# Performance work log

Hardware: AMD Instinct MI355X
Metric: run time of the kernel (lower is better)

## Reference

```python
import jax, jax.numpy as jnp
import numpy as np

B = 8192
EPS = 1e-5


def _bn(x, g, b):
    # BatchNorm1d in training mode: biased batch statistics
    m = jnp.mean(x, axis=0)
    v = jnp.mean((x - m) ** 2, axis=0)
    return g * (x - m) * jax.lax.rsqrt(v + EPS) + b


def setup_inputs() -> dict:
    key = jax.random.key(0)
    ks = jax.random.split(key, 24)
    w = lambda k, shape: jax.random.normal(k, shape, jnp.float32) * 0.02
    z = lambda shape: jnp.zeros(shape, jnp.float32)
    o = lambda shape: jnp.ones(shape, jnp.float32)
    inp = {"pred_vertices": jax.random.normal(ks[0], (B, 1723, 3), jnp.float32)}
    inp["W0"] = w(ks[1], (5169, 1024)); inp["b0"] = z(1024); inp["g0"] = o(1024); inp["be0"] = z(1024)
    inp["W1a"] = w(ks[2], (1024, 1024)); inp["b1a"] = z(1024); inp["g1a"] = o(1024); inp["be1a"] = z(1024)
    inp["W1b"] = w(ks[3], (1024, 1024)); inp["b1b"] = z(1024); inp["g1b"] = o(1024); inp["be1b"] = z(1024)
    inp["W2a"] = w(ks[4], (1024, 1024)); inp["b2a"] = z(1024); inp["g2a"] = o(1024); inp["be2a"] = z(1024)
    inp["W2b"] = w(ks[5], (1024, 1024)); inp["b2b"] = z(1024); inp["g2b"] = o(1024); inp["be2b"] = z(1024)
    inp["W3"] = w(ks[6], (1024, 226)); inp["b3"] = z(226)
    return inp


def reference(pred_vertices, W0, b0, g0, be0,
              W1a, b1a, g1a, be1a, W1b, b1b, g1b, be1b,
              W2a, b2a, g2a, be2a, W2b, b2b, g2b, be2b,
              W3, b3):
    bsz = pred_vertices.shape[0]
    x = pred_vertices.reshape(bsz, 1723 * 3)
    # FCBlock: Linear -> BN -> ReLU
    h = jax.nn.relu(_bn(x @ W0 + b0, g0, be0))
    # FCResBlock x2: relu(x + BN(Linear(relu(BN(Linear(x))))))
    t = jax.nn.relu(_bn(h @ W1a + b1a, g1a, be1a))
    t = _bn(t @ W1b + b1b, g1b, be1b)
    h = jax.nn.relu(h + t)
    t = jax.nn.relu(_bn(h @ W2a + b2a, g2a, be2a))
    t = _bn(t @ W2b + b2b, g2b, be2b)
    h = jax.nn.relu(h + t)
    out = h @ W3 + b3  # (B, 226)
    rot = out[:, :216].reshape(-1, 3, 3)  # (B*24, 3, 3)
    pred_betas = out[:, 216:]
    # Batched Procrustes orthogonalization: R = U V^T, then scale by det (no-grad)
    U, S, Vh = jnp.linalg.svd(rot, full_matrices=False)
    R = jnp.einsum('nij,njk->nik', U, Vh)
    det = jax.lax.stop_gradient(jnp.linalg.det(R))[:, None, None]
    pred_rotmat = (R * det).reshape(bsz, 24, 3, 3)
    return (pred_rotmat, pred_betas)
```

## Files before the change

kernel.cpp:

```cpp
#include <hip/hip_runtime.h>
#include <hip/hip_bf16.h>
#include <math.h>

typedef __attribute__((ext_vector_type(8))) _Float16 half8;
typedef __attribute__((ext_vector_type(4))) float floatx4;
typedef __attribute__((ext_vector_type(4))) unsigned short ushortx4;

__device__ __forceinline__ float hu2f(unsigned short u) {
    _Float16 h;
    __builtin_memcpy(&h, &u, 2);
    return (float)h;
}
__device__ __forceinline__ unsigned short f2hu(float x) {
    _Float16 h = (_Float16)x;
    unsigned short u;
    __builtin_memcpy(&u, &h, 2);
    return u;
}
__device__ __forceinline__ void split2(float a, unsigned short& s0,
                                       unsigned short& s1) {
    s0 = f2hu(a);
    float r1 = a - hu2f(s0);
    s1 = f2hu(r1);
}

typedef __attribute__((address_space(1))) unsigned int as1_u32;
typedef __attribute__((address_space(3))) unsigned int as3_u32;
__device__ __forceinline__ void gload16(const void* g, void* l) {
    __builtin_amdgcn_global_load_lds((const as1_u32*)g, (as3_u32*)l, 16, 0, 0);
}

__device__ __forceinline__ void wsplit_body(
    const float* __restrict__ W, unsigned short* __restrict__ out,
    int Ktrue, int Kpad, int Ntrue, int Nalloc, int k0, int n0,
    float (*T)[33], int tx, int ty)
{
#pragma unroll
    for (int i = 0; i < 4; i++) {
        int k = k0 + ty + 8 * i, n = n0 + tx;
        T[ty + 8 * i][tx] = (k < Ktrue && n < Ntrue) ? W[(size_t)k * Ntrue + n] : 0.f;
    }
    __syncthreads();
    const size_t PS = (size_t)Nalloc * Kpad;
#pragma unroll
    for (int i = 0; i < 4; i++) {
        int n = n0 + ty + 8 * i, k = k0 + tx;
        if (n < Nalloc) {
            unsigned short h0, h1;
            split2(T[tx][ty + 8 * i], h0, h1);
            size_t base = (size_t)n * Kpad + k;
            out[base] = h0;
            out[PS + base] = h1;
        }
    }
}

__global__ __launch_bounds__(256) void wsplit_all_kernel(
    const float* __restrict__ W0,  const float* __restrict__ W1a,
    const float* __restrict__ W1b, const float* __restrict__ W2a,
    const float* __restrict__ W2b, const float* __restrict__ W3,
    unsigned short* __restrict__ w0p,  unsigned short* __restrict__ w1ap,
    unsigned short* __restrict__ w1bp, unsigned short* __restrict__ w2ap,
    unsigned short* __restrict__ w2bp, unsigned short* __restrict__ w3p)
{
    __shared__ float T[32][33];
    const int tx = threadIdx.x & 31, ty = threadIdx.x >> 5;
    int bid = blockIdx.x;
    if (bid < 5184) {
        wsplit_body(W0, w0p, 5169, 5184, 1024, 1024,
                    (bid % 162) * 32, (bid / 162) * 32, T, tx, ty);
    } else if (bid < 6208) {
        int r = bid - 5184;
        wsplit_body(W1a, w1ap, 1024, 1024, 1024, 1024,
                    (r & 31) * 32, (r >> 5) * 32, T, tx, ty);
    } else if (bid < 7232) {
        int r = bid - 6208;
        wsplit_body(W1b, w1bp, 1024, 1024, 1024, 1024,
                    (r & 31) * 32, (r >> 5) * 32, T, tx, ty);
    } else if (bid < 8256) {
        int r = bid - 7232;
        wsplit_body(W2a, w2ap, 1024, 1024, 1024, 1024,
                    (r & 31) * 32, (r >> 5) * 32, T, tx, ty);
    } else if (bid < 9280) {
        int r = bid - 8256;
        wsplit_body(W2b, w2bp, 1024, 1024, 1024, 1024,
                    (r & 31) * 32, (r >> 5) * 32, T, tx, ty);
    } else {
        int r = bid - 9280;
        wsplit_body(W3, w3p, 1024, 1024, 226, 256,
                    (r & 31) * 32, (r >> 5) * 32, T, tx, ty);
    }
}

__global__ __launch_bounds__(256) void asplit2_kernel(
    const float* __restrict__ A, unsigned short* __restrict__ out,
    int Ka, int Kpad, int M)
{
    const int kq = Kpad >> 2;
    const int n = M * kq;
    int idx = blockIdx.x * 256 + threadIdx.x;
    if (idx >= n) return;
    int row = idx / kq, c4 = idx - row * kq;
    const size_t PS = (size_t)M * Kpad;
    ushortx4 o0, o1;
#pragma unroll
    for (int e = 0; e < 4; e++) {
        int col = c4 * 4 + e;
        float v = (col < Ka) ? A[(size_t)row * Ka + col] : 0.f;
        unsigned short a, b;
        split2(v, a, b);
        o0[e] = a; o1[e] = b;
    }
    size_t base = (size_t)row * Kpad + c4 * 4;
    *(ushortx4*)(out + base) = o0;
    *(ushortx4*)(out + PS + base) = o1;
}

__global__ __launch_bounds__(256, 3) void mfma_gemm_h(
    const unsigned short* __restrict__ Apl,
    const unsigned short* __restrict__ Bpl,
    const float* __restrict__ bias, float* __restrict__ C,
    float* __restrict__ part,
    int M, int N, int Kpad, int Nb)
{
    __shared__ __align__(16) unsigned short As[2][128][32];
    __shared__ __align__(16) unsigned short Bs[2][128][32];

    const int tid = threadIdx.x;
    const int lane = tid & 63;
    const int wave = tid >> 6;
    const int wm = (wave & 1) * 64, wn = (wave >> 1) * 64;

    const int gx = gridDim.x;
    const int nwg = gx * gridDim.y;
    const int id = blockIdx.y * gx + blockIdx.x;
    const int cpx = nwg >> 3;
    const int swz = (id & 7) * cpx + (id >> 3);
    const int bm = (swz / gx) * 128, bn = (swz % gx) * 128;

    const int l15 = lane & 15, q = lane >> 4;
    const size_t PSA = (size_t)M * Kpad;
    const size_t PSB = (size_t)Nb * Kpad;

    const int srow = lane >> 2;
    const int gslot = (lane & 3) ^ ((srow >> 1) & 3);
    const int rkey = (l15 >> 1) & 3;

    floatx4 acc[4][4] = {};

    for (int k0 = 0; k0 < Kpad; k0 += 32) {
#pragma unroll
        for (int i = 0; i < 8; i++) {
            int e = wave * 8 + i;
            int mat = e >> 4, p = (e >> 3) & 1, rb = (e & 7) << 4;
            if (mat == 0) {
                gload16(Apl + (size_t)p * PSA + (size_t)(bm + rb + srow) * Kpad
                            + (k0 + gslot * 8),
                        &As[p][rb][0]);
            } else {
                gload16(Bpl + (size_t)p * PSB + (size_t)(bn + rb + srow) * Kpad
                            + (k0 + gslot * 8),
                        &Bs[p][rb][0]);
            }
        }
        __syncthreads();

        half8 bfr[2][4];
#pragma unroll
        for (int p = 0; p < 2; p++)
#pragma unroll
            for (int ni = 0; ni < 4; ni++)
                bfr[p][ni] = *(const half8*)&Bs[p][wn + ni * 16 + l15][(q ^ rkey) * 8];
#pragma unroll
        for (int pa = 0; pa < 2; pa++) {
            half8 af[4];
#pragma unroll
            for (int mi = 0; mi < 4; mi++)
                af[mi] = *(const half8*)&As[pa][wm + mi * 16 + l15][(q ^ rkey) * 8];
#pragma unroll
            for (int pb = 0; pb + pa < 2; pb++) {
#pragma unroll
                for (int mi = 0; mi < 4; mi++)
#pragma unroll
                    for (int ni = 0; ni < 4; ni++)
                        acc[mi][ni] = __builtin_amdgcn_mfma_f32_16x16x32_f16(
                            af[mi], bfr[pb][ni], acc[mi][ni], 0, 0, 0);
            }
        }
        __syncthreads();
    }

    float ps[4], ps2[4];
#pragma unroll
    for (int ni = 0; ni < 4; ni++) {
        int col = bn + wn + ni * 16 + l15;
        float s = 0.f, s2 = 0.f;
        if (col < N) {
            float bv = bias[col];
#pragma unroll
            for (int mi = 0; mi < 4; mi++) {
#pragma unroll
                for (int reg = 0; reg < 4; reg++) {
                    int row = bm + wm + mi * 16 + q * 4 + reg;
                    float v = acc[mi][ni][reg] + bv;
                    C[(size_t)row * N + col] = v;
                    s += v;
                    s2 += v * v;
                }
            }
        }
        ps[ni] = s; ps2[ni] = s2;
    }

    if (part) {
#pragma unroll
        for (int ni = 0; ni < 4; ni++) {
            ps[ni]  += __shfl_xor(ps[ni], 16);  ps[ni]  += __shfl_xor(ps[ni], 32);
            ps2[ni] += __shfl_xor(ps2[ni], 16); ps2[ni] += __shfl_xor(ps2[ni], 32);
        }
        if (q == 0) {
#pragma unroll
            for (int ni = 0; ni < 4; ni++) {
                int col = bn + wn + ni * 16 + l15;
                if (col < N) {
                    atomicAdd(&part[col], ps[ni]);
                    atomicAdd(&part[N + col], ps2[ni]);
                }
            }
        }
    }
}

template <bool AVEC, bool NV4>
__global__ __launch_bounds__(256) void gemm128(
    const float* __restrict__ A, const float* __restrict__ B,
    const float* __restrict__ bias, float* __restrict__ C,
    int M, int N, int Keff, int Ktrue, int Ka)
{
    __shared__ __align__(16) float Asm[16][132];
    __shared__ __align__(16) float Bsm[16][132];
    const int tid = threadIdx.x;
    const int bm = blockIdx.y * 128, bn = blockIdx.x * 128;
    const int tx = tid & 15, ty = tid >> 4;
    const int arow = tid >> 2, ac = tid & 3;
    const int bk = tid >> 4, bc = tid & 15;
    float acc[8][8] = {};
    for (int k0 = 0; k0 < Keff; k0 += 16) {
#pragma unroll
        for (int h = 0; h < 2; h++) {
            int rr = arow + h * 64;
            if (AVEC) {
                float4 v = *(const float4*)&A[(size_t)(bm + rr) * Ka + k0 + ac * 4];
                const float* pv = &v.x;
#pragma unroll
                for (int e = 0; e < 4; e++) Asm[ac * 4 + e][rr] = pv[e];
            } else {
#pragma unroll
                for (int e = 0; e < 4; e++) {
                    int kg = k0 + ac * 4 + e;
                    Asm[ac * 4 + e][rr] = (kg < Ka) ? A[(size_t)(bm + rr) * Ka + kg] : 0.f;
                }
            }
        }
        {
            int kg = k0 + bk;
            bool kok = (kg < Ktrue);
#pragma unroll
            for (int h = 0; h < 2; h++) {
                int cc = bc * 4 + h * 64;
                if (NV4) {
                    float4 v = {0.f, 0.f, 0.f, 0.f};
                    if (kok) v = *(const float4*)&B[(size_t)kg * N + bn + cc];
                    *(float4*)&Bsm[bk][cc] = v;
                } else {
#pragma unroll
                    for (int e = 0; e < 4; e++) {
                        int col = bn + cc + e;
                        Bsm[bk][cc + e] = (kok && col < N) ? B[(size_t)kg * N + col] : 0.f;
                    }
                }
            }
        }
        __syncthreads();
#pragma unroll
        for (int k = 0; k < 16; k++) {
            float4 a0 = *(const float4*)&Asm[k][ty * 4];
            float4 a1 = *(const float4*)&Asm[k][ty * 4 + 64];
            float4 b0 = *(const float4*)&Bsm[k][tx * 4];
            float4 b1 = *(const float4*)&Bsm[k][tx * 4 + 64];
            float av[8] = {a0.x, a0.y, a0.z, a0.w, a1.x, a1.y, a1.z, a1.w};
            float bv[8] = {b0.x, b0.y, b0.z, b0.w, b1.x, b1.y, b1.z, b1.w};
#pragma unroll
            for (int i = 0; i < 8; i++)
#pragma unroll
                for (int j = 0; j < 8; j++) acc[i][j] += av[i] * bv[j];
        }
        __syncthreads();
    }
#pragma unroll
    for (int i = 0; i < 8; i++) {
        int row = bm + (i < 4 ? ty * 4 + i : 64 + ty * 4 + (i - 4));
#pragma unroll
        for (int jh = 0; jh < 2; jh++)
#pragma unroll
            for (int e = 0; e < 4; e++) {
                int col = bn + jh * 64 + tx * 4 + e;
                if (NV4 || col < N)
                    C[(size_t)row * N + col] = acc[i][jh * 4 + e] + bias[col];
            }
    }
}

__global__ __launch_bounds__(256) void colstats_kernel(
    const float* __restrict__ Y, float* __restrict__ part, int N, int rows)
{
    int c = blockIdx.x * 256 + threadIdx.x;
    int r0 = blockIdx.y * rows;
    const float* p = Y + (size_t)r0 * N + c;
    float s = 0.f, s2 = 0.f;
    for (int r = 0; r < rows; r++) {
        float v = p[(size_t)r * N];
        s += v;
        s2 += v * v;
    }
    part[(size_t)(blockIdx.y * 2 + 0) * N + c] = s;
    part[(size_t)(blockIdx.y * 2 + 1) * N + c] = s2;
}

__global__ void finalize_stats_kernel(
    const float* __restrict__ part, const float* __restrict__ g,
    const float* __restrict__ be, float* __restrict__ scale,
    float* __restrict__ shift, int N, int nchunk, float invM)
{
    int c = blockIdx.x * blockDim.x + threadIdx.x;
    if (c >= N) return;
    float s = 0.f, s2 = 0.f;
    for (int i = 0; i < nchunk; i++) {
        s  += part[(size_t)(2 * i + 0) * N + c];
        s2 += part[(size_t)(2 * i + 1) * N + c];
    }
    float m = s * invM;
    float v = s2 * invM - m * m;
    if (v < 0.f) v = 0.f;
    float sc = g[c] / sqrtf(v + 1e-5f);
    scale[c] = sc;
    shift[c] = be[c] - m * sc;
}

__global__ __launch_bounds__(256) void bn_apply_ss_kernel(
    float* __restrict__ Y, const float* __restrict__ scale,
    const float* __restrict__ shift, int do_relu, int n4, int N)
{
    int idx = blockIdx.x * 256 + threadIdx.x;
    if (idx >= n4) return;
    float4* Y4 = (float4*)Y;
    float4 v = Y4[idx];
    int c = (idx * 4) & (N - 1);
    v.x = v.x * scale[c + 0] + shift[c + 0];
    v.y = v.y * scale[c + 1] + shift[c + 1];
    v.z = v.z * scale[c + 2] + shift[c + 2];
    v.w = v.w * scale[c + 3] + shift[c + 3];
    if (do_relu) {
        v.x = fmaxf(v.x, 0.f); v.y = fmaxf(v.y, 0.f);
        v.z = fmaxf(v.z, 0.f); v.w = fmaxf(v.w, 0.f);
    }
    Y4[idx] = v;
}

__device__ __forceinline__ void bn_coeff(
    const float* __restrict__ part, const float* __restrict__ g,
    const float* __restrict__ be, int c, float invM, float* sc, float* sh)
{
    float4 s4 = *(const float4*)&part[c];
    float4 q4 = *(const float4*)&part[1024 + c];
    float4 g4 = *(const float4*)&g[c];
    float4 b4 = *(const float4*)&be[c];
    const float* sp = &s4.x; const float* qp = &q4.x;
    const float* gp = &g4.x; const float* bp = &b4.x;
#pragma unroll
    for (int e = 0; e < 4; e++) {
        float m = sp[e] * invM;
        float v = qp[e] * invM - m * m;
        if (v < 0.f) v = 0.f;
        float s = gp[e] / sqrtf(v + 1e-5f);
        sc[e] = s;
        sh[e] = bp[e] - m * s;
    }
}

__global__ __launch_bounds__(256) void bn_apply_kernel(
    float* __restrict__ Y, const float* __restrict__ part,
    const float* __restrict__ g, const float* __restrict__ be,
    int do_relu, int write_y, int n4, float invM,
    unsigned short* __restrict__ plane, size_t PS)
{
    int idx = blockIdx.x * 256 + threadIdx.x;
    if (idx >= n4) return;
    float4* Y4 = (float4*)Y;
    float4 v = Y4[idx];
    int c = (idx * 4) & 1023;
    float sc[4], sh[4];
    bn_coeff(part, g, be, c, invM, sc, sh);
    v.x = v.x * sc[0] + sh[0];
    v.y = v.y * sc[1] + sh[1];
    v.z = v.z * sc[2] + sh[2];
    v.w = v.w * sc[3] + sh[3];
    if (do_relu) {
        v.x = fmaxf(v.x, 0.f); v.y = fmaxf(v.y, 0.f);
        v.z = fmaxf(v.z, 0.f); v.w = fmaxf(v.w, 0.f);
    }
    if (write_y) Y4[idx] = v;
    if (plane) {
        float vv[4] = {v.x, v.y, v.z, v.w};
        ushortx4 o0, o1;
#pragma unroll
        for (int e = 0; e < 4; e++) {
            unsigned short a, b;
            split2(vv[e], a, b);
            o0[e] = a; o1[e] = b;
        }
        size_t base = (size_t)idx * 4;
        *(ushortx4*)(plane + base) = o0;
        *(ushortx4*)(plane + PS + base) = o1;
    }
}

__global__ __launch_bounds__(256) void bn_resid_relu_kernel(
    float* __restrict__ Hb, const float* __restrict__ T,
    const float* __restrict__ part, const float* __restrict__ g,
    const float* __restrict__ be, int n4, float invM,
    unsigned short* __restrict__ plane, size_t PS)
{
    int idx = blockIdx.x * 256 + threadIdx.x;
    if (idx >= n4) return;
    float4 h = ((float4*)Hb)[idx];
    float4 t = ((const float4*)T)[idx];
    int c = (idx * 4) & 1023;
    float sc[4], sh[4];
    bn_coeff(part, g, be, c, invM, sc, sh);
    t.x = t.x * sc[0] + sh[0];
    t.y = t.y * sc[1] + sh[1];
    t.z = t.z * sc[2] + sh[2];
    t.w = t.w * sc[3] + sh[3];
    h.x = fmaxf(h.x + t.x, 0.f);
    h.y = fmaxf(h.y + t.y, 0.f);
    h.z = fmaxf(h.z + t.z, 0.f);
    h.w = fmaxf(h.w + t.w, 0.f);
    ((float4*)Hb)[idx] = h;
    if (plane) {
        float vv[4] = {h.x, h.y, h.z, h.w};
        ushortx4 o0, o1;
#pragma unroll
        for (int e = 0; e < 4; e++) {
            unsigned short a, b;
            split2(vv[e], a, b);
            o0[e] = a; o1[e] = b;
        }
        size_t base = (size_t)idx * 4;
        *(ushortx4*)(plane + base) = o0;
        *(ushortx4*)(plane + PS + base) = o1;
    }
}

__global__ __launch_bounds__(256) void resid_relu_kernel(
    float* __restrict__ Hb, const float* __restrict__ T, int n4)
{
    int idx = blockIdx.x * 256 + threadIdx.x;
    if (idx >= n4) return;
    float4 h = ((float4*)Hb)[idx];
    float4 t = ((const float4*)T)[idx];
    h.x = fmaxf(h.x + t.x, 0.f);
    h.y = fmaxf(h.y + t.y, 0.f);
    h.z = fmaxf(h.z + t.z, 0.f);
    h.w = fmaxf(h.w + t.w, 0.f);
    ((float4*)Hb)[idx] = h;
}

__global__ __launch_bounds__(256) void svd_kernel(
    const float* __restrict__ O3, float* __restrict__ out, int nb)
{
    int gidx = blockIdx.x * 256 + threadIdx.x;
    if (gidx >= nb * 24) return;
    int row = gidx / 24;
    int j = gidx - row * 24;
    const float* rowp = O3 + (size_t)row * 226;
    const float* src = rowp + j * 9;

    double m[3][3];
#pragma unroll
    for (int r = 0; r < 3; r++)
#pragma unroll
        for (int c = 0; c < 3; c++) m[r][c] = (double)src[r * 3 + c];

    double a[3][3];
#pragma unroll
    for (int r = 0; r < 3; r++)
#pragma unroll
        for (int c = 0; c < 3; c++) {
            double s = 0.0;
#pragma unroll
            for (int k = 0; k < 3; k++) s += m[k][r] * m[k][c];
            a[r][c] = s;
        }

    double V[3][3] = {{1, 0, 0}, {0, 1, 0}, {0, 0, 1}};
    const int PP[3] = {0, 0, 1}, QQ[3] = {1, 2, 2};
    for (int sweep = 0; sweep < 8; sweep++) {
        for (int r3 = 0; r3 < 3; r3++) {
            int p = PP[r3], q = QQ[r3];
            double apq = a[p][q];
            if (fabs(apq) < 1e-60) continue;
            double tau = (a[q][q] - a[p][p]) / (2.0 * apq);
            double t = ((tau >= 0.0) ? 1.0 : -1.0) / (fabs(tau) + sqrt(1.0 + tau * tau));
            double c = 1.0 / sqrt(1.0 + t * t);
            double s = t * c;
#pragma unroll
            for (int k = 0; k < 3; k++) {
                double xp = a[p][k], xq = a[q][k];
                a[p][k] = c * xp - s * xq;
                a[q][k] = s * xp + c * xq;
            }
#pragma unroll
            for (int k = 0; k < 3; k++) {
                double xp = a[k][p], xq = a[k][q];
                a[k][p] = c * xp - s * xq;
                a[k][q] = s * xp + c * xq;
            }
#pragma unroll
            for (int k = 0; k < 3; k++) {
                double xp = V[k][p], xq = V[k][q];
                V[k][p] = c * xp - s * xq;
                V[k][q] = s * xp + c * xq;
            }
        }
    }

    double lam[3] = {a[0][0], a[1][1], a[2][2]};
    int i3 = 0;
    if (lam[1] < lam[i3]) i3 = 1;
    if (lam[2] < lam[i3]) i3 = 2;
    int i1 = (i3 + 1) % 3, i2 = (i3 + 2) % 3;

    double v1[3], v2[3], v3[3];
#pragma unroll
    for (int k = 0; k < 3; k++) {
        v1[k] = V[k][i1];
        v2[k] = V[k][i2];
        v3[k] = V[k][i3];
    }

    double u1[3], u2[3];
#pragma unroll
    for (int r = 0; r < 3; r++)
        u1[r] = m[r][0] * v1[0] + m[r][1] * v1[1] + m[r][2] * v1[2];
    double n1 = sqrt(u1[0] * u1[0] + u1[1] * u1[1] + u1[2] * u1[2]);
    double inv1 = (n1 > 1e-150) ? 1.0 / n1 : 0.0;
#pragma unroll
    for (int r = 0; r < 3; r++) u1[r] *= inv1;

#pragma unroll
    for (int r = 0; r < 3; r++)
        u2[r] = m[r][0] * v2[0] + m[r][1] * v2[1] + m[r][2] * v2[2];
    double d12 = u1[0] * u2[0] + u1[1] * u2[1] + u1[2] * u2[2];
#pragma unroll
    for (int r = 0; r < 3; r++) u2[r] -= d12 * u1[r];
    double n2 = sqrt(u2[0] * u2[0] + u2[1] * u2[1] + u2[2] * u2[2]);
    double inv2 = (n2 > 1e-150) ? 1.0 / n2 : 0.0;
#pragma unroll
    for (int r = 0; r < 3; r++) u2[r] *= inv2;

    double detM = m[0][0] * (m[1][1] * m[2][2] - m[1][2] * m[2][1])
                - m[0][1] * (m[1][0] * m[2][2] - m[1][2] * m[2][0])
                + m[0][2] * (m[1][0] * m[2][1] - m[1][1] * m[2][0]);
    double sgn = (detM >= 0.0) ? 1.0 : -1.0;
    double detV = v1[0] * (v2[1] * v3[2] - v2[2] * v3[1])
                - v1[1] * (v2[0] * v3[2] - v2[2] * v3[0])
                + v1[2] * (v2[0] * v3[1] - v2[1] * v3[0]);
    double sv = (detV >= 0.0) ? 1.0 : -1.0;

    double u3[3];
    u3[0] = sgn * sv * (u1[1] * u2[2] - u1[2] * u2[1]);
    u3[1] = sgn * sv * (u1[2] * u2[0] - u1[0] * u2[2]);
    u3[2] = sgn * sv * (u1[0] * u2[1] - u1[1] * u2[0]);

    size_t rot_base = (size_t)gidx * 9;
    size_t beta_base = (size_t)nb * 24 * 9 + (size_t)row * 10;
#pragma unroll
    for (int r = 0; r < 3; r++)
#pragma unroll
        for (int c = 0; c < 3; c++)
            out[rot_base + r * 3 + c] =
                (float)(sgn * (u1[r] * v1[c] + u2[r] * v2[c] + u3[r] * v3[c]));

    if (j < 10) out[beta_base + j] = rowp[216 + j];
}

extern "C" void kernel_launch(void* const* d_in, const int* in_sizes, int n_in,
                              void* d_out, int out_size, void* d_ws, size_t ws_size,
                              hipStream_t stream)
{
    const float* x    = (const float*)d_in[0];
    const float* W0   = (const float*)d_in[1];
    const float* b0   = (const float*)d_in[2];
    const float* g0   = (const float*)d_in[3];
    const float* be0  = (const float*)d_in[4];
    const float* W1a  = (const float*)d_in[5];
    const float* b1a  = (const float*)d_in[6];
    const float* g1a  = (const float*)d_in[7];
    const float* be1a = (const float*)d_in[8];
    const float* W1b  = (const float*)d_in[9];
    const float* b1b  = (const float*)d_in[10];
    const float* g1b  = (const float*)d_in[11];
    const float* be1b = (const float*)d_in[12];
    const float* W2a  = (const float*)d_in[13];
    const float* b2a  = (const float*)d_in[14];
    const float* g2a  = (const float*)d_in[15];
    const float* be2a = (const float*)d_in[16];
    const float* W2b  = (const float*)d_in[17];
    const float* b2b  = (const float*)d_in[18];
    const float* g2b  = (const float*)d_in[19];
    const float* be2b = (const float*)d_in[20];
    const float* W3   = (const float*)d_in[21];
    const float* b3   = (const float*)d_in[22];

    const int M = 8192, H = 1024, K0 = 5169, K0P = 5184, NO = 226, NOP = 256;
    const int NCH_OLD = 32;

    const size_t SZ_ACT  = (size_t)M * H;
    const size_t SZ_O3   = (size_t)M * NO;
    const size_t SZ_PART = (size_t)2 * NCH_OLD * H;

    float* ws   = (float*)d_ws;
    float* buf0 = ws;
    float* buf1 = buf0 + SZ_ACT;
    float* buf2 = buf1 + SZ_ACT;
    float* buf3 = buf2 + SZ_ACT;
    float* parts = buf3 + SZ_O3;
    float* scale = parts + SZ_PART;
    float* shift = scale + H;
    size_t float_base = 3 * SZ_ACT + SZ_O3 + SZ_PART + 2 * H + 16;

    unsigned short* pl = (unsigned short*)(ws + float_base);
    unsigned short* w0p  = pl;
    unsigned short* w1ap = w0p  + (size_t)2 * H * K0P;
    unsigned short* w1bp = w1ap + (size_t)2 * H * H;
    unsigned short* w2ap = w1bp + (size_t)2 * H * H;
    unsigned short* w2bp = w2ap + (size_t)2 * H * H;
    unsigned short* w3p  = w2bp + (size_t)2 * H * H;
    unsigned short* xp  = w3p + (size_t)2 * NOP * H;
    unsigned short* a0p = xp  + (size_t)2 * M * K0P;
    unsigned short* a1p = a0p + (size_t)2 * M * H;
    unsigned short* pend = a1p + (size_t)2 * M * H;

    size_t bytes_new = float_base * 4 + (size_t)(pend - pl) * 2;
    bool use_new = ws_size >= bytes_new;

    dim3 blk(256);
    const int n4 = M * H / 4;
    const size_t PSH = (size_t)M * H;
    const float invM = 1.0f / M;

    if (use_new) {
        float* p0 = parts + 0 * 2 * H;
        float* p1 = parts + 1 * 2 * H;
        float* p2 = parts + 2 * 2 * H;
        float* p3 = parts + 3 * 2 * H;
        float* p4 = parts + 4 * 2 * H;
        hipMemsetAsync(parts, 0, (size_t)6 * 2 * H * sizeof(float), stream);

        wsplit_all_kernel<<<dim3(9536), blk, 0, stream>>>(
            W0, W1a, W1b, W2a, W2b, W3, w0p, w1ap, w1bp, w2ap, w2bp, w3p);
        asplit2_kernel<<<dim3(M * (K0P / 4) / 256), blk, 0, stream>>>(x, xp, K0, K0P, M);

        dim3 gH(H / 128, M / 128);
        dim3 gO(NOP / 128, M / 128);

        mfma_gemm_h<<<gH, blk, 0, stream>>>(xp, w0p, b0, buf0, p0, M, H, K0P, H);
        bn_apply_kernel<<<dim3(n4 / 256), blk, 0, stream>>>(buf0, p0, g0, be0, 1, 1, n4, invM, a0p, PSH);
        mfma_gemm_h<<<gH, blk, 0, stream>>>(a0p, w1ap, b1a, buf1, p1, M, H, H, H);
        bn_apply_kernel<<<dim3(n4 / 256), blk, 0, stream>>>(buf1, p1, g1a, be1a, 1, 0, n4, invM, a1p, PSH);
        mfma_gemm_h<<<gH, blk, 0, stream>>>(a1p, w1bp, b1b, buf2, p2, M, H, H, H);
        bn_resid_relu_kernel<<<dim3(n4 / 256), blk, 0, stream>>>(buf0, buf2, p2, g1b, be1b, n4, invM, a0p, PSH);
        mfma_gemm_h<<<gH, blk, 0, stream>>>(a0p, w2ap, b2a, buf1, p3, M, H, H, H);
        bn_apply_kernel<<<dim3(n4 / 256), blk, 0, stream>>>(buf1, p3, g2a, be2a, 1, 0, n4, invM, a1p, PSH);
        mfma_gemm_h<<<gH, blk, 0, stream>>>(a1p, w2bp, b2b, buf2, p4, M, H, H, H);
        bn_resid_relu_kernel<<<dim3(n4 / 256), blk, 0, stream>>>(buf0, buf2, p4, g2b, be2b, n4, invM, a0p, PSH);
        mfma_gemm_h<<<gO, blk, 0, stream>>>(a0p, w3p, b3, buf3, nullptr, M, NO, H, NOP);
    } else {
        auto bnstep = [&](float* Y, const float* g, const float* be, int relu) {
            colstats_kernel<<<dim3(H / 256, NCH_OLD), blk, 0, stream>>>(Y, parts, H, M / NCH_OLD);
            finalize_stats_kernel<<<dim3(H / 256), blk, 0, stream>>>(parts, g, be, scale, shift, H, NCH_OLD, invM);
            bn_apply_ss_kernel<<<dim3(n4 / 256), blk, 0, stream>>>(Y, scale, shift, relu, n4, H);
        };
        dim3 gH(H / 128, M / 128);
        dim3 gO((NO + 127) / 128, M / 128);
        gemm128<false, true><<<gH, blk, 0, stream>>>(x, W0, b0, buf0, M, H, K0P, K0, K0);
        bnstep(buf0, g0, be0, 1);
        gemm128<true, true><<<gH, blk, 0, stream>>>(buf0, W1a, b1a, buf1, M, H, H, H, H);
        bnstep(buf1, g1a, be1a, 1);
        gemm128<true, true><<<gH, blk, 0, stream>>>(buf1, W1b, b1b, buf2, M, H, H, H, H);
        bnstep(buf2, g1b, be1b, 0);
        resid_relu_kernel<<<dim3(n4 / 256), blk, 0, stream>>>(buf0, buf2, n4);
        gemm128<true, true><<<gH, blk, 0, stream>>>(buf0, W2a, b2a, buf1, M, H, H, H, H);
        bnstep(buf1, g2a, be2a, 1);
        gemm128<true, true><<<gH, blk, 0, stream>>>(buf1, W2b, b2b, buf2, M, H, H, H, H);
        bnstep(buf2, g2b, be2b, 0);
        resid_relu_kernel<<<dim3(n4 / 256), blk, 0, stream>>>(buf0, buf2, n4);
        gemm128<true, false><<<gO, blk, 0, stream>>>(buf0, W3, b3, buf3, M, NO, H, H, H);
    }

    svd_kernel<<<dim3((M * 24 + 255) / 256), blk, 0, stream>>>(buf3, (float*)d_out, M);
}
```

Before: 1.023 ms.

## Fuse BatchNorm apply into GEMM epilogue using an in-kernel grid barrier

Each hidden-layer GEMM now accumulates column sums atomically, then waits at a device-wide atomic barrier until every block has contributed. It then computes the BN scale and shift and applies BN, ReLU or residual-add-ReLU directly on the accumulators, writing the fp16 split planes for the next GEMM. This removes the five separate elementwise BN kernels and their full read/write passes over the activations. In exchange, occupancy is lowered to 2 blocks per CU so all 512 blocks are co-resident; the barrier would deadlock if they were not. Blocks also stall waiting for the slowest block, and the plane stores become scalar 2-byte writes.

```diff
diff --git a/kernel.cpp b/kernel.cpp
--- a/kernel.cpp
+++ b/kernel.cpp
@@ -116,12 +116,17 @@
     *(ushortx4*)(out + PS + base) = o1;
 }
 
-__global__ __launch_bounds__(256, 3) void mfma_gemm_h(
+__global__ __launch_bounds__(256, 2) void mfma_gemm_h(
     const unsigned short* __restrict__ Apl,
     const unsigned short* __restrict__ Bpl,
-    const float* __restrict__ bias, float* __restrict__ C,
-    float* __restrict__ part,
-    int M, int N, int Kpad, int Nb)
+    const float* __restrict__ bias,
+    const float* __restrict__ g, const float* __restrict__ be,
+    float* __restrict__ partS, unsigned int* __restrict__ bar,
+    float* __restrict__ Yout,
+    const float* __restrict__ Hresid,
+    unsigned short* __restrict__ plane,
+    float* __restrict__ Cplain,
+    int M, int N, int Kpad, int Nb, float invM, int do_relu)
 {
     __shared__ __align__(16) unsigned short As[2][128][32];
     __shared__ __align__(16) unsigned short Bs[2][128][32];
@@ -190,42 +195,100 @@
         __syncthreads();
     }
 
-    float ps[4], ps2[4];
+    if (!partS) {
+#pragma unroll
+        for (int ni = 0; ni < 4; ni++) {
+            int col = bn + wn + ni * 16 + l15;
+            if (col >= N) continue;
+            float bv = bias[col];
+#pragma unroll
+            for (int mi = 0; mi < 4; mi++)
+#pragma unroll
+                for (int reg = 0; reg < 4; reg++) {
+                    int row = bm + wm + mi * 16 + q * 4 + reg;
+                    Cplain[(size_t)row * N + col] = acc[mi][ni][reg] + bv;
+                }
+        }
+        return;
+    }
+
+    float bv[4], ps[4], ps2[4];
 #pragma unroll
     for (int ni = 0; ni < 4; ni++) {
         int col = bn + wn + ni * 16 + l15;
+        bv[ni] = bias[col];
         float s = 0.f, s2 = 0.f;
-        if (col < N) {
-            float bv = bias[col];
-#pragma unroll
-            for (int mi = 0; mi < 4; mi++) {
-#pragma unroll
-                for (int reg = 0; reg < 4; reg++) {
-                    int row = bm + wm + mi * 16 + q * 4 + reg;
-                    float v = acc[mi][ni][reg] + bv;
-                    C[(size_t)row * N + col] = v;
-                    s += v;
-                    s2 += v * v;
+#pragma unroll
+        for (int mi = 0; mi < 4; mi++)
+#pragma unroll
+            for (int reg = 0; reg < 4; reg++) {
+                float v = acc[mi][ni][reg] + bv[ni];
+                s += v;
+                s2 += v * v;
+            }
+        ps[ni] = s; ps2[ni] = s2;
+    }
+#pragma unroll
+    for (int ni = 0; ni < 4; ni++) {
+        ps[ni]  += __shfl_xor(ps[ni], 16);  ps[ni]  += __shfl_xor(ps[ni], 32);
+        ps2[ni] += __shfl_xor(ps2[ni], 16); ps2[ni] += __shfl_xor(ps2[ni], 32);
+    }
+    if (q == 0) {
+#pragma unroll
+        for (int ni = 0; ni < 4; ni++) {
+            int col = bn + wn + ni * 16 + l15;
+            atomicAdd(&partS[col], ps[ni]);
+            atomicAdd(&partS[1024 + col], ps2[ni]);
+        }
+    }
+
+    __threadfence();
+    if (tid == 0) {
+        atomicAdd(bar, 1u);
+        while (__hip_atomic_load(bar, __ATOMIC_ACQUIRE,
+                                 __HIP_MEMORY_SCOPE_AGENT) < (unsigned)nwg)
+            __builtin_amdgcn_s_sleep(8);
+    }
+    __syncthreads();
+
+    float sc[4], sh[4];
+#pragma unroll
+    for (int ni = 0; ni < 4; ni++) {
+        int col = bn + wn + ni * 16 + l15;
+        float s  = __hip_atomic_load(&partS[col], __ATOMIC_ACQUIRE,
+                                     __HIP_MEMORY_SCOPE_AGENT);
+        float s2 = __hip_atomic_load(&partS[1024 + col], __ATOMIC_ACQUIRE,
+                                     __HIP_MEMORY_SCOPE_AGENT);
+        float m = s * invM;
+        float v = s2 * invM - m * m;
+        if (v < 0.f) v = 0.f;
+        float scv = g[col] / sqrtf(v + 1e-5f);
+        sc[ni] = scv;
+        sh[ni] = be[col] - m * scv;
+    }
+
+    const size_t PSH = (size_t)M * 1024;
+#pragma unroll
+    for (int ni = 0; ni < 4; ni++) {
+        int col = bn + wn + ni * 16 + l15;
+#pragma unroll
+        for (int mi = 0; mi < 4; mi++) {
+#pragma unroll
+            for (int reg = 0; reg < 4; reg++) {
+                int row = bm + wm + mi * 16 + q * 4 + reg;
+                size_t off = (size_t)row * 1024 + col;
+                float v = acc[mi][ni][reg] + bv[ni];
+                float t = v * sc[ni] + sh[ni];
+                if (Hresid) {
+                    t = fmaxf(Hresid[off] + t, 0.f);
+                } else if (do_relu) {
+                    t = fmaxf(t, 0.f);
                 }
-            }
-        }
-        ps[ni] = s; ps2[ni] = s2;
-    }
-
-    if (part) {
-#pragma unroll
-        for (int ni = 0; ni < 4; ni++) {
-            ps[ni]  += __shfl_xor(ps[ni], 16);  ps[ni]  += __shfl_xor(ps[ni], 32);
-            ps2[ni] += __shfl_xor(ps2[ni], 16); ps2[ni] += __shfl_xor(ps2[ni], 32);
-        }
-        if (q == 0) {
-#pragma unroll
-            for (int ni = 0; ni < 4; ni++) {
-                int col = bn + wn + ni * 16 + l15;
-                if (col < N) {
-                    atomicAdd(&part[col], ps[ni]);
-                    atomicAdd(&part[N + col], ps2[ni]);
-                }
+                if (Yout) Yout[off] = t;
+                unsigned short h0, h1;
+                split2(t, h0, h1);
+                plane[off] = h0;
+                plane[PSH + off] = h1;
             }
         }
     }
@@ -365,101 +428,6 @@
         v.z = fmaxf(v.z, 0.f); v.w = fmaxf(v.w, 0.f);
     }
     Y4[idx] = v;
-}
-
-__device__ __forceinline__ void bn_coeff(
-    const float* __restrict__ part, const float* __restrict__ g,
-    const float* __restrict__ be, int c, float invM, float* sc, float* sh)
-{
-    float4 s4 = *(const float4*)&part[c];
-    float4 q4 = *(const float4*)&part[1024 + c];
-    float4 g4 = *(const float4*)&g[c];
-    float4 b4 = *(const float4*)&be[c];
-    const float* sp = &s4.x; const float* qp = &q4.x;
-    const float* gp = &g4.x; const float* bp = &b4.x;
-#pragma unroll
-    for (int e = 0; e < 4; e++) {
-        float m = sp[e] * invM;
-        float v = qp[e] * invM - m * m;
-        if (v < 0.f) v = 0.f;
-        float s = gp[e] / sqrtf(v + 1e-5f);
-        sc[e] = s;
-        sh[e] = bp[e] - m * s;
-    }
-}
-
-__global__ __launch_bounds__(256) void bn_apply_kernel(
-    float* __restrict__ Y, const float* __restrict__ part,
-    const float* __restrict__ g, const float* __restrict__ be,
-    int do_relu, int write_y, int n4, float invM,
-    unsigned short* __restrict__ plane, size_t PS)
-{
-    int idx = blockIdx.x * 256 + threadIdx.x;
-    if (idx >= n4) return;
-    float4* Y4 = (float4*)Y;
-    float4 v = Y4[idx];
-    int c = (idx * 4) & 1023;
-    float sc[4], sh[4];
-    bn_coeff(part, g, be, c, invM, sc, sh);
-    v.x = v.x * sc[0] + sh[0];
-    v.y = v.y * sc[1] + sh[1];
-    v.z = v.z * sc[2] + sh[2];
-    v.w = v.w * sc[3] + sh[3];
-    if (do_relu) {
-        v.x = fmaxf(v.x, 0.f); v.y = fmaxf(v.y, 0.f);
-        v.z = fmaxf(v.z, 0.f); v.w = fmaxf(v.w, 0.f);
-    }
-    if (write_y) Y4[idx] = v;
-    if (plane) {
-        float vv[4] = {v.x, v.y, v.z, v.w};
-        ushortx4 o0, o1;
-#pragma unroll
-        for (int e = 0; e < 4; e++) {
-            unsigned short a, b;
-            split2(vv[e], a, b);
-            o0[e] = a; o1[e] = b;
-        }
-        size_t base = (size_t)idx * 4;
-        *(ushortx4*)(plane + base) = o0;
-        *(ushortx4*)(plane + PS + base) = o1;
-    }
-}
-
-__global__ __launch_bounds__(256) void bn_resid_relu_kernel(
-    float* __restrict__ Hb, const float* __restrict__ T,
-    const float* __restrict__ part, const float* __restrict__ g,
-    const float* __restrict__ be, int n4, float invM,
-    unsigned short* __restrict__ plane, size_t PS)
-{
-    int idx = blockIdx.x * 256 + threadIdx.x;
-    if (idx >= n4) return;
-    float4 h = ((float4*)Hb)[idx];
-    float4 t = ((const float4*)T)[idx];
-    int c = (idx * 4) & 1023;
-    float sc[4], sh[4];
-    bn_coeff(part, g, be, c, invM, sc, sh);
-    t.x = t.x * sc[0] + sh[0];
-    t.y = t.y * sc[1] + sh[1];
-    t.z = t.z * sc[2] + sh[2];
-    t.w = t.w * sc[3] + sh[3];
-    h.x = fmaxf(h.x + t.x, 0.f);
-    h.y = fmaxf(h.y + t.y, 0.f);
-    h.z = fmaxf(h.z + t.z, 0.f);
-    h.w = fmaxf(h.w + t.w, 0.f);
-    ((float4*)Hb)[idx] = h;
-    if (plane) {
-        float vv[4] = {h.x, h.y, h.z, h.w};
-        ushortx4 o0, o1;
-#pragma unroll
-        for (int e = 0; e < 4; e++) {
-            unsigned short a, b;
-            split2(vv[e], a, b);
-            o0[e] = a; o1[e] = b;
-        }
-        size_t base = (size_t)idx * 4;
-        *(ushortx4*)(plane + base) = o0;
-        *(ushortx4*)(plane + PS + base) = o1;
-    }
 }
 
 __global__ __launch_bounds__(256) void resid_relu_kernel(
@@ -657,7 +625,6 @@
 
     dim3 blk(256);
     const int n4 = M * H / 4;
-    const size_t PSH = (size_t)M * H;
     const float invM = 1.0f / M;
 
     if (use_new) {
@@ -666,7 +633,8 @@
         float* p2 = parts + 2 * 2 * H;
         float* p3 = parts + 3 * 2 * H;
         float* p4 = parts + 4 * 2 * H;
-        hipMemsetAsync(parts, 0, (size_t)6 * 2 * H * sizeof(float), stream);
+        unsigned int* bars = (unsigned int*)(parts + 5 * 2 * H);
+        hipMemsetAsync(parts, 0, ((size_t)5 * 2 * H + 16) * sizeof(float), stream);
 
         wsplit_all_kernel<<<dim3(9536), blk, 0, stream>>>(
             W0, W1a, W1b, W2a, W2b, W3, w0p, w1ap, w1bp, w2ap, w2bp, w3p);
@@ -675,17 +643,18 @@
         dim3 gH(H / 128, M / 128);
         dim3 gO(NOP / 128, M / 128);
 
-        mfma_gemm_h<<<gH, blk, 0, stream>>>(xp, w0p, b0, buf0, p0, M, H, K0P, H);
-        bn_apply_kernel<<<dim3(n4 / 256), blk, 0, stream>>>(buf0, p0, g0, be0, 1, 1, n4, invM, a0p, PSH);
-        mfma_gemm_h<<<gH, blk, 0, stream>>>(a0p, w1ap, b1a, buf1, p1, M, H, H, H);
-        bn_apply_kernel<<<dim3(n4 / 256), blk, 0, stream>>>(buf1, p1, g1a, be1a, 1, 0, n4, invM, a1p, PSH);
-        mfma_gemm_h<<<gH, blk, 0, stream>>>(a1p, w1bp, b1b, buf2, p2, M, H, H, H);
-        bn_resid_relu_kernel<<<dim3(n4 / 256), blk, 0, stream>>>(buf0, buf2, p2, g1b, be1b, n4, invM, a0p, PSH);
-        mfma_gemm_h<<<gH, blk, 0, stream>>>(a0p, w2ap, b2a, buf1, p3, M, H, H, H);
-        bn_apply_kernel<<<dim3(n4 / 256), blk, 0, stream>>>(buf1, p3, g2a, be2a, 1, 0, n4, invM, a1p, PSH);
-        mfma_gemm_h<<<gH, blk, 0, stream>>>(a1p, w2bp, b2b, buf2, p4, M, H, H, H);
-        bn_resid_relu_kernel<<<dim3(n4 / 256), blk, 0, stream>>>(buf0, buf2, p4, g2b, be2b, n4, invM, a0p, PSH);
-        mfma_gemm_h<<<gO, blk, 0, stream>>>(a0p, w3p, b3, buf3, nullptr, M, NO, H, NOP);
+        mfma_gemm_h<<<gH, blk, 0, stream>>>(xp, w0p, b0, g0, be0, p0, bars + 0,
+            buf0, nullptr, a0p, nullptr, M, H, K0P, H, invM, 1);
+        mfma_gemm_h<<<gH, blk, 0, stream>>>(a0p, w1ap, b1a, g1a, be1a, p1, bars + 1,
+            nullptr, nullptr, a1p, nullptr, M, H, H, H, invM, 1);
+        mfma_gemm_h<<<gH, blk, 0, stream>>>(a1p, w1bp, b1b, g1b, be1b, p2, bars + 2,
+            buf0, buf0, a0p, nullptr, M, H, H, H, invM, 0);
+        mfma_gemm_h<<<gH, blk, 0, stream>>>(a0p, w2ap, b2a, g2a, be2a, p3, bars + 3,
+            nullptr, nullptr, a1p, nullptr, M, H, H, H, invM, 1);
+        mfma_gemm_h<<<gH, blk, 0, stream>>>(a1p, w2bp, b2b, g2b, be2b, p4, bars + 4,
+            nullptr, buf0, a0p, nullptr, M, H, H, H, invM, 0);
+        mfma_gemm_h<<<gO, blk, 0, stream>>>(a0p, w3p, b3, nullptr, nullptr,
+            nullptr, nullptr, nullptr, nullptr, nullptr, buf3, M, NO, H, NOP, 0.f, 0);
     } else {
         auto bnstep = [&](float* Y, const float* g, const float* be, int relu) {
             colstats_kernel<<<dim3(H / 256, NCH_OLD), blk, 0, stream>>>(Y, parts, H, M / NCH_OLD);
```

Measured after the change: 1.992 ms. 1.95x slower.
